# Kernel tuning notes

Measured on AMD Instinct MI355X. Metric: run time of the kernel, lower is better.

Reference implementation:

```python
import jax, jax.numpy as jnp
import numpy as np

DIM, H, C = 1024, 16, 64
D = DIM // H  # head_dim = 64
GATE_HID = 16


def setup_inputs() -> dict:
    key = jax.random.key(0)
    ks = jax.random.split(key, 8)
    B, L = 2, 2048

    def xav(k, fan_in, fan_out):
        return jax.random.normal(k, (fan_in, fan_out), jnp.float32) * np.sqrt(2.0 / (fan_in + fan_out))

    return {
        "x": jax.random.normal(ks[0], (B, L, DIM), jnp.float32),
        "Wq": xav(ks[1], DIM, DIM), "bq": jnp.zeros((DIM,), jnp.float32),
        "Wk": xav(ks[2], DIM, DIM), "bk": jnp.zeros((DIM,), jnp.float32),
        "Wv": xav(ks[3], DIM, DIM), "bv": jnp.zeros((DIM,), jnp.float32),
        "Wg1": xav(ks[4], DIM, GATE_HID), "bg1": jnp.zeros((GATE_HID,), jnp.float32),
        "Wg2": xav(ks[5], GATE_HID, H * D), "bg2": jnp.zeros((H * D,), jnp.float32),
    }


def reference(x, Wq, bq, Wk, bk, Wv, bv, Wg1, bg1, Wg2, bg2):
    B, L, dim = x.shape
    pad = (-L) % C
    if pad:
        x = jnp.pad(x, ((0, 0), (0, pad), (0, 0)))
    Lp = L + pad

    def proj(W, b):
        # (B, Lp, dim) -> (B, H, Lp, D)
        return (x @ W + b).reshape(B, Lp, H, D).transpose(0, 2, 1, 3)

    q, k, v = proj(Wq, bq), proj(Wk, bk), proj(Wv, bv)
    gate = jax.nn.sigmoid(jax.nn.silu(x @ Wg1 + bg1) @ Wg2 + bg2)
    alpha = 0.9 * gate.reshape(B, Lp, H, D).transpose(0, 2, 1, 3) + 0.1  # (B,H,Lp,D)

    # --- intra-chunk causal softmax attention (vectorized over chunks) ---
    Nc = Lp // C
    qc = q.reshape(B, H, Nc, C, D)
    kc = k.reshape(B, H, Nc, C, D)
    vc = v.reshape(B, H, Nc, C, D)
    scores = jnp.einsum('bhncd,bhnkd->bhnck', qc, kc) / np.sqrt(D).astype(np.float32)
    causal = jnp.tril(jnp.ones((C, C), bool))
    scores = jnp.where(causal, scores, -jnp.inf)
    intra = jnp.einsum('bhnck,bhnke->bhnce', jax.nn.softmax(scores, axis=-1), vc)
    intra = intra.reshape(B, H, Lp, D)

    # --- inter: gated linear-attention recurrence over the full sequence ---
    # Note: in the original code S is updated every timestep (including inside
    # chunks), so the 'inter' term at step t sees ALL tokens < t, not just
    # previous chunks.
    def step(S, inp):
        q_t, k_t, v_t, a_t = inp  # each (B, H, D)
        inter_t = jnp.einsum('bhd,bhde->bhe', q_t, S)
        S = a_t[..., None] * S + k_t[..., None] * v_t[..., None, :]
        return S, inter_t

    xs = tuple(a.transpose(2, 0, 1, 3) for a in (q, k, v, alpha))  # (Lp, B, H, D)
    S0 = jnp.zeros((B, H, D, D), x.dtype)
    _, inter = jax.lax.scan(step, S0, xs)  # (Lp, B, H, D)
    inter = inter.transpose(1, 2, 0, 3)  # (B, H, Lp, D)

    out = (inter + intra).transpose(0, 2, 1, 3).reshape(B, Lp, dim)
    return out[:, :L]
```

## Files before the change

### kernel.cpp

```cpp
#include <hip/hip_runtime.h>
#include <math.h>

#define DIMN 1024
#define NH 16
#define HD 64
#define CHK 64
#define NB 2
#define SEQ 2048
#define NTOK (NB*SEQ)
#define NCHUNK (SEQ/CHK)
#define GH 16

typedef __bf16 bf16x8 __attribute__((ext_vector_type(8)));
typedef float f32x4 __attribute__((ext_vector_type(4)));
typedef unsigned short u16x4 __attribute__((ext_vector_type(4)));

__device__ __forceinline__ unsigned short f2bf(float f) {
  union { float f; unsigned u; } a; a.f = f;
  unsigned r = a.u + 0x7FFFu + ((a.u >> 16) & 1u);
  return (unsigned short)(r >> 16);
}
__device__ __forceinline__ float bf2f(unsigned short v) {
  union { unsigned u; float f; } a; a.u = ((unsigned)v) << 16;
  return a.f;
}

__device__ __forceinline__ void gload16(const void* g, void* l) {
  __builtin_amdgcn_global_load_lds(
      (const __attribute__((address_space(1))) void*)g,
      (__attribute__((address_space(3))) void*)l, 16, 0, 0);
}

__global__ __launch_bounds__(256) void k_cast_wT(const float* __restrict__ W0,
    const float* __restrict__ W1, const float* __restrict__ W2,
    unsigned short* __restrict__ wt) {
  __shared__ float tile[64][68];
  int z = blockIdx.z;
  const float* W = z==0 ? W0 : z==1 ? W1 : W2;
  unsigned short* o = wt + (size_t)z*DIMN*DIMN;
  int k0 = blockIdx.y*64, n0 = blockIdx.x*64;
  int tr = threadIdx.x >> 4, c0 = (threadIdx.x & 15)*4;
  #pragma unroll
  for (int s = 0; s < 4; ++s) {
    int r = tr + s*16;
    *(f32x4*)&tile[r][c0] = *(const f32x4*)(W + (size_t)(k0+r)*DIMN + n0 + c0);
  }
  __syncthreads();
  #pragma unroll
  for (int s = 0; s < 4; ++s) {
    int nn = tr + s*16;
    ushort4 v;
    v.x = f2bf(tile[c0+0][nn]);
    v.y = f2bf(tile[c0+1][nn]);
    v.z = f2bf(tile[c0+2][nn]);
    v.w = f2bf(tile[c0+3][nn]);
    *(ushort4*)(o + (size_t)(n0+nn)*DIMN + k0 + c0) = v;
  }
}

__global__ __launch_bounds__(256) void k_wg1t(const float* __restrict__ Wg1,
    unsigned short* __restrict__ wg1b) {
  int idx = blockIdx.x*256 + threadIdx.x;
  int k = idx & 1023, j = idx >> 10;
  wg1b[j*DIMN + k] = f2bf(Wg1[k*GH + j]);
}

__global__ __launch_bounds__(256) void k_castx_hidden(const float* __restrict__ x,
    const unsigned short* __restrict__ wg1b, const float* __restrict__ bg1,
    unsigned short* __restrict__ xb, float* __restrict__ hid) {
  __shared__ __align__(16) unsigned short xs[16][1032];
  __shared__ float red[4][16][16];
  int tid = threadIdx.x;
  size_t base = (size_t)blockIdx.x * 16 * DIMN;
  #pragma unroll
  for (int i = 0; i < 16; ++i) {
    int idx4 = tid + i*256;
    int r = idx4 >> 8, c4 = idx4 & 255;
    f32x4 v = *(const f32x4*)(x + base + (size_t)idx4*4);
    u16x4 o;
    o[0]=f2bf(v[0]); o[1]=f2bf(v[1]); o[2]=f2bf(v[2]); o[3]=f2bf(v[3]);
    *(u16x4*)&xs[r][c4*4] = o;
    *(u16x4*)(xb + base + (size_t)idx4*4) = o;
  }
  __syncthreads();
  int l = tid & 63, w = tid >> 6;
  int lr = l & 15, kg = l >> 4;
  union FB { uint4 u; bf16x8 h; } a, b;
  f32x4 acc = {0.f,0.f,0.f,0.f};
  const unsigned short* wrow = wg1b + (size_t)lr*DIMN + w*256 + kg*8;
  #pragma unroll
  for (int kk = 0; kk < 8; ++kk) {
    a.u = *(const uint4*)&xs[lr][w*256 + kk*32 + kg*8];
    b.u = *(const uint4*)(wrow + kk*32);
    acc = __builtin_amdgcn_mfma_f32_16x16x32_bf16(a.h, b.h, acc, 0, 0, 0);
  }
  #pragma unroll
  for (int rg = 0; rg < 4; ++rg) red[w][kg*4 + rg][lr] = acc[rg];
  __syncthreads();
  {
    int m = tid >> 4, j = tid & 15;
    float s = red[0][m][j] + red[1][m][j] + red[2][m][j] + red[3][m][j];
    s += bg1[j];
    hid[(blockIdx.x*16 + m)*GH + j] = s / (1.f + expf(-s));
  }
}

__global__ __launch_bounds__(256) void k_projqkv(const unsigned short* __restrict__ xb,
    const unsigned short* __restrict__ wt,
    const float* __restrict__ b0, const float* __restrict__ b1, const float* __restrict__ b2,
    unsigned short* __restrict__ o0, unsigned short* __restrict__ o1,
    unsigned short* __restrict__ o2) {
  __shared__ unsigned short As[2][128*32];
  __shared__ unsigned short Bs[2][128*32];
  int tid = threadIdx.x;
  int wg = blockIdx.y * gridDim.x + blockIdx.x;
  int swz = (wg & 7) * 96 + (wg >> 3);
  int bx = swz % 24, by = swz / 24;
  int n3 = bx*128;
  int z = n3 >> 10;
  int n0l = n3 & 1023;
  const float* bias = z==0 ? b0 : z==1 ? b1 : b2;
  unsigned short* out = z==0 ? o0 : z==1 ? o1 : o2;
  int m0 = by*128;

  int l = tid & 63;
  int w = tid >> 6;
  int wr = w >> 1, wc = w & 1;
  int lrow = l & 15, kg = l >> 4;

  f32x4 acc[4][4] = {};

  int r0s = tid >> 2, s0s = tid & 3;
  int r1s = (tid + 256) >> 2;
  int sg0 = s0s ^ ((r0s >> 1) & 3);
  int sg1 = s0s ^ ((r1s >> 1) & 3);

  #define STAGE(buf, kt) do { \
    int kb_ = (kt)*32; \
    gload16(xb + ((size_t)(m0 + r0s)*DIMN + kb_ + sg0*8), &As[buf][tid*8]); \
    gload16(wt + ((size_t)(n3 + r0s)*DIMN + kb_ + sg0*8), &Bs[buf][tid*8]); \
    gload16(xb + ((size_t)(m0 + r1s)*DIMN + kb_ + sg1*8), &As[buf][(tid+256)*8]); \
    gload16(wt + ((size_t)(n3 + r1s)*DIMN + kb_ + sg1*8), &Bs[buf][(tid+256)*8]); \
  } while (0)

  STAGE(0, 0);
  int buf = 0;
  for (int t = 0; t < DIMN/32; ++t) {
    __syncthreads();
    if (t+1 < DIMN/32) STAGE(buf^1, t+1);
    union { uint4 u; bf16x8 h; } af[4], bfr[4];
    #pragma unroll
    for (int mf = 0; mf < 4; ++mf) {
      int r = wr*64 + mf*16 + lrow;
      int slot = kg ^ ((r >> 1) & 3);
      af[mf].u = *(const uint4*)&As[buf][r*32 + slot*8];
    }
    #pragma unroll
    for (int nf = 0; nf < 4; ++nf) {
      int r = wc*64 + nf*16 + lrow;
      int slot = kg ^ ((r >> 1) & 3);
      bfr[nf].u = *(const uint4*)&Bs[buf][r*32 + slot*8];
    }
    #pragma unroll
    for (int mf = 0; mf < 4; ++mf)
      #pragma unroll
      for (int nf = 0; nf < 4; ++nf)
        acc[mf][nf] = __builtin_amdgcn_mfma_f32_16x16x32_bf16(
            af[mf].h, bfr[nf].h, acc[mf][nf], 0, 0, 0);
    buf ^= 1;
  }
  #undef STAGE

  float bv[4];
  #pragma unroll
  for (int nf = 0; nf < 4; ++nf) bv[nf] = bias[n0l + wc*64 + nf*16 + lrow];
  #pragma unroll
  for (int mf = 0; mf < 4; ++mf) {
    int rbase = m0 + wr*64 + mf*16 + kg*4;
    #pragma unroll
    for (int nf = 0; nf < 4; ++nf) {
      int c = n0l + wc*64 + nf*16 + lrow;
      #pragma unroll
      for (int rg = 0; rg < 4; ++rg)
        out[(size_t)(rbase+rg)*DIMN + c] = f2bf(acc[mf][nf][rg] + bv[nf]);
    }
  }
}

__global__ __launch_bounds__(256) void k_ginc(const unsigned short* __restrict__ kbuf,
    const unsigned short* __restrict__ vbuf,
    const float* __restrict__ hid, const float* __restrict__ Wg2,
    const float* __restrict__ bg2,
    unsigned short* __restrict__ G, float* __restrict__ Bv) {
  __shared__ __align__(16) float kl[CHK][HD+4];
  __shared__ __align__(16) float vl[CHK][HD+4];
  __shared__ __align__(16) float al[CHK][HD+4];
  __shared__ float wprod[4][HD];
  int tid = threadIdx.x;
  int bid = blockIdx.x;
  int bh = bid >> 5, n = bid & 31;
  int b = bh >> 4, h = bh & 15;
  int colbase = h*HD;
  size_t rowbase = (size_t)b*SEQ + n*CHK;
  int dd = tid & 63, w = tid >> 6;

  float* scr = &al[0][0];
  {
    int r = tid >> 2, j0 = (tid & 3)*4;
    *(f32x4*)&scr[r*16 + j0] = *(const f32x4*)(hid + (rowbase + r)*GH + j0);
    int j = tid >> 4, d0 = (tid & 15)*4;
    *(f32x4*)&scr[1024 + j*64 + d0] = *(const f32x4*)(Wg2 + (size_t)j*DIMN + colbase + d0);
  }
  #pragma unroll
  for (int i = 0; i < 4; ++i) {
    int f4 = tid + i*256;
    int r = f4 >> 4, cg = f4 & 15;
    size_t g = (rowbase + r)*DIMN + colbase + cg*4;
    u16x4 k4 = *(const u16x4*)(kbuf + g);
    u16x4 v4 = *(const u16x4*)(vbuf + g);
    #pragma unroll
    for (int j = 0; j < 4; ++j) {
      kl[r][cg*4+j] = bf2f(k4[j]);
      vl[r][cg*4+j] = bf2f(v4[j]);
    }
  }
  __syncthreads();

  float av[16];
  {
    int r = tid >> 2, db = (tid & 3)*16;
    #pragma unroll
    for (int dq = 0; dq < 16; ++dq) {
      int d = db + dq;
      float acc = bg2[colbase + d];
      #pragma unroll
      for (int j = 0; j < GH; ++j)
        acc = fmaf(scr[r*16 + j], scr[1024 + j*64 + d], acc);
      float gg = 1.f/(1.f + expf(-acc));
      av[dq] = fmaf(0.9f, gg, 0.1f);
    }
  }
  __syncthreads();
  {
    int r = tid >> 2, db = (tid & 3)*16;
    #pragma unroll
    for (int dq = 0; dq < 16; dq += 4) {
      f32x4 v4 = {av[dq], av[dq+1], av[dq+2], av[dq+3]};
      *(f32x4*)&al[r][db + dq] = v4;
    }
  }
  __syncthreads();

  {
    float sp = 1.f;
    for (int ii = 15; ii >= 0; --ii) {
      int i = w*16 + ii;
      kl[i][dd] *= sp;
      sp *= al[i][dd];
    }
    wprod[w][dd] = sp;
  }
  __syncthreads();
  if (w < 3) {
    float tail = 1.f;
    for (int w2 = w+1; w2 < 4; ++w2) tail *= wprod[w2][dd];
    for (int ii = 0; ii < 16; ++ii) kl[w*16+ii][dd] *= tail;
  }
  if (tid < HD)
    Bv[(size_t)bid*HD + tid] = wprod[0][tid]*wprod[1][tid]*wprod[2][tid]*wprod[3][tid];
  __syncthreads();

  int ti = tid >> 4, te = tid & 15;
  int d0 = ti*4, e0 = te*4;
  float acc[4][4] = {};
  for (int i = 0; i < CHK; ++i) {
    float4 kh = *(const float4*)&kl[i][d0];
    float4 vv = *(const float4*)&vl[i][e0];
    float kf[4] = {kh.x,kh.y,kh.z,kh.w};
    float vf[4] = {vv.x,vv.y,vv.z,vv.w};
    #pragma unroll
    for (int r = 0; r < 4; ++r)
      #pragma unroll
      for (int c = 0; c < 4; ++c)
        acc[r][c] = fmaf(kf[r], vf[c], acc[r][c]);
  }
  unsigned short* gp = G + (size_t)bid*(HD*HD);
  #pragma unroll
  for (int r = 0; r < 4; ++r) {
    ushort4 o;
    o.x = f2bf(acc[r][0]); o.y = f2bf(acc[r][1]);
    o.z = f2bf(acc[r][2]); o.w = f2bf(acc[r][3]);
    *(ushort4*)(gp + (d0+r)*HD + e0) = o;
  }
}

__global__ __launch_bounds__(256) void k_scan(unsigned short* __restrict__ buf,
    const float* __restrict__ Bv) {
  int idx = blockIdx.x*256 + threadIdx.x;
  int e = idx & 63, d = (idx >> 6) & 63, bh = idx >> 12;
  unsigned short* gp = buf + (size_t)bh*NCHUNK*HD*HD + d*HD + e;
  const float* bp = Bv + (size_t)bh*NCHUNK*HD + d;
  float s = 0.f;
  float g = bf2f(gp[0]), bb = bp[0];
  #pragma unroll
  for (int n = 0; n < NCHUNK; ++n) {
    float gn = 0.f, bn = 0.f;
    if (n+1 < NCHUNK) { gn = bf2f(gp[(n+1)*(HD*HD)]); bn = bp[(n+1)*HD]; }
    gp[n*(HD*HD)] = f2bf(s);
    s = fmaf(bb, s, g);
    g = gn; bb = bn;
  }
}

__global__ __launch_bounds__(256) void k_chunk(const unsigned short* __restrict__ qbuf,
    const unsigned short* __restrict__ kbuf, const unsigned short* __restrict__ vbuf,
    const float* __restrict__ hid, const float* __restrict__ Wg2,
    const float* __restrict__ bg2,
    const unsigned short* __restrict__ states, float* __restrict__ outp) {
  __shared__ __align__(16) unsigned short qb16[64*72];
  __shared__ __align__(16) unsigned short kb16[64*72];
  __shared__ __align__(16) unsigned short vT[64*72];
  __shared__ __align__(16) unsigned short Pl[64*72];
  __shared__ __align__(16) unsigned short Swt[2][64*72];
  __shared__ __align__(16) float lb[65*68];
  __shared__ __align__(16) unsigned short dgs[4][16*40];
  __shared__ float seg[4][64];

  const int tid = threadIdx.x;
  const int bid = blockIdx.x;
  const int bh = bid >> 5, n = bid & 31;
  const int b = bh >> 4, h = bh & 15;
  const int colbase = h*HD;
  const size_t rowbase = (size_t)b*SEQ + n*CHK;
  const unsigned short* stp = states + (size_t)(bh*NCHUNK + n)*(HD*HD);

  float* scr = (float*)Pl;
  {
    int r = tid >> 2, j0 = (tid & 3)*4;
    *(f32x4*)&scr[r*16 + j0] = *(const f32x4*)(hid + (rowbase + r)*GH + j0);
    int j = tid >> 4, d0 = (tid & 15)*4;
    *(f32x4*)&scr[1024 + j*64 + d0] = *(const f32x4*)(Wg2 + (size_t)j*DIMN + colbase + d0);
  }
  #pragma unroll
  for (int i = 0; i < 4; ++i) {
    int f4 = tid + i*256;
    int r = f4 >> 4, cg = f4 & 15, c0 = cg*4;
    size_t g = (rowbase + r)*DIMN + colbase + c0;
    u16x4 q4 = *(const u16x4*)(qbuf + g);
    u16x4 k4 = *(const u16x4*)(kbuf + g);
    u16x4 v4 = *(const u16x4*)(vbuf + g);
    u16x4 s4 = *(const u16x4*)(stp + r*HD + c0);
    #pragma unroll
    for (int j = 0; j < 4; ++j) {
      vT[(c0+j)*72 + r] = v4[j];
      Swt[0][(c0+j)*72 + r] = s4[j];
    }
    *(u16x4*)&qb16[r*72 + c0] = q4;
    *(u16x4*)&kb16[r*72 + c0] = k4;
  }
  __syncthreads();

  {
    int r = tid >> 2, db = (tid & 3)*16;
    float av[16];
    #pragma unroll
    for (int dq = 0; dq < 16; ++dq) {
      int d = db + dq;
      float acc = bg2[colbase + d];
      #pragma unroll
      for (int j = 0; j < GH; ++j)
        acc = fmaf(scr[r*16 + j], scr[1024 + j*64 + d], acc);
      float gg = 1.f/(1.f + expf(-acc));
      av[dq] = log2f(fmaf(0.9f, gg, 0.1f));
    }
    #pragma unroll
    for (int dq = 0; dq < 16; dq += 4) {
      f32x4 v4 = {av[dq], av[dq+1], av[dq+2], av[dq+3]};
      *(f32x4*)&lb[r*68 + db + dq] = v4;
    }
  }
  __syncthreads();

  {
    int d = tid & 63, ww = tid >> 6;
    float run = 0.f;
    #pragma unroll
    for (int ii = 0; ii < 16; ++ii) {
      int i = ww*16 + ii;
      float t = lb[i*68 + d];
      lb[i*68 + d] = run;
      run += t;
    }
    seg[ww][d] = run;
  }
  __syncthreads();
  {
    int d = tid & 63, ww = tid >> 6;
    float carry = 0.f;
    for (int w2 = 0; w2 < ww; ++w2) carry += seg[w2][d];
    if (ww > 0)
      for (int ii = 0; ii < 16; ++ii) lb[(ww*16+ii)*68 + d] += carry;
    if (ww == 3) lb[64*68 + d] = carry + seg[3][d];
  }
  __syncthreads();

  const int l = tid & 63, w = tid >> 6;
  const int lr = l & 15, lg = l >> 4;
  const int ks = lg*8;
  const int arow = w*16 + lr;

  union FB { uint4 u; bf16x8 h; unsigned short s[8]; };

  FB qa0, qa1;
  qa0.u = *(const uint4*)&qb16[arow*72 + ks];
  qa1.u = *(const uint4*)&qb16[arow*72 + 32 + ks];
  f32x4 sc[4];
  #pragma unroll
  for (int nf = 0; nf < 4; ++nf) {
    FB b0, b1;
    b0.u = *(const uint4*)&kb16[(nf*16+lr)*72 + ks];
    b1.u = *(const uint4*)&kb16[(nf*16+lr)*72 + 32 + ks];
    f32x4 z = {0.f,0.f,0.f,0.f};
    z = __builtin_amdgcn_mfma_f32_16x16x32_bf16(qa0.h, b0.h, z, 0,0,0);
    z = __builtin_amdgcn_mfma_f32_16x16x32_bf16(qa1.h, b1.h, z, 0,0,0);
    sc[nf] = z;
  }

  float rmax[4] = {-3e38f,-3e38f,-3e38f,-3e38f};
  #pragma unroll
  for (int nf = 0; nf < 4; ++nf) {
    int col = nf*16 + lr;
    #pragma unroll
    for (int rg = 0; rg < 4; ++rg) {
      int row = w*16 + lg*4 + rg;
      float v = sc[nf][rg]*0.125f;
      if (col > row) v = -1e30f;
      sc[nf][rg] = v;
      rmax[rg] = fmaxf(rmax[rg], v);
    }
  }
  #pragma unroll
  for (int m = 1; m <= 8; m <<= 1)
    #pragma unroll
    for (int rg = 0; rg < 4; ++rg)
      rmax[rg] = fmaxf(rmax[rg], __shfl_xor(rmax[rg], m));
  float rsum[4] = {0.f,0.f,0.f,0.f};
  #pragma unroll
  for (int nf = 0; nf < 4; ++nf)
    #pragma unroll
    for (int rg = 0; rg < 4; ++rg) {
      float e = exp2f((sc[nf][rg] - rmax[rg])*1.44269504f);
      sc[nf][rg] = e;
      rsum[rg] += e;
    }
  #pragma unroll
  for (int m = 1; m <= 8; m <<= 1)
    #pragma unroll
    for (int rg = 0; rg < 4; ++rg)
      rsum[rg] += __shfl_xor(rsum[rg], m);
  __syncthreads();
  #pragma unroll
  for (int nf = 0; nf < 4; ++nf)
    #pragma unroll
    for (int rg = 0; rg < 4; ++rg)
      Pl[(w*16 + lg*4 + rg)*72 + nf*16 + lr] = f2bf(sc[nf][rg]);
  float inv[4];
  #pragma unroll
  for (int rg = 0; rg < 4; ++rg) inv[rg] = 1.f/rsum[rg];
  __syncthreads();

  f32x4 acc[4];
  {
    FB p0, p1;
    p0.u = *(const uint4*)&Pl[arow*72 + ks];
    p1.u = *(const uint4*)&Pl[arow*72 + 32 + ks];
    #pragma unroll
    for (int nf = 0; nf < 4; ++nf) {
      FB v0, v1;
      v0.u = *(const uint4*)&vT[(nf*16+lr)*72 + ks];
      v1.u = *(const uint4*)&vT[(nf*16+lr)*72 + 32 + ks];
      f32x4 z = {0.f,0.f,0.f,0.f};
      z = __builtin_amdgcn_mfma_f32_16x16x32_bf16(p0.h, v0.h, z, 0,0,0);
      z = __builtin_amdgcn_mfma_f32_16x16x32_bf16(p1.h, v1.h, z, 0,0,0);
      #pragma unroll
      for (int rg = 0; rg < 4; ++rg)
        acc[nf][rg] = z[rg]*inv[rg];
    }
  }

  {
    int dA = arow;
    float lb32 = lb[32*68 + dA];
    FB ku;
    #pragma unroll
    for (int j = 0; j < 8; ++j) {
      int s = ks + j;
      float kv = bf2f(kb16[s*72 + dA]);
      ku.s[j] = f2bf(kv * exp2f(lb32 - lb[(s+1)*68 + dA]));
    }
    int d0 = w*16 + lg*4;
    float bs[4];
    #pragma unroll
    for (int rg = 0; rg < 4; ++rg) bs[rg] = exp2f(lb[32*68 + d0 + rg]);
    #pragma unroll
    for (int nf = 0; nf < 4; ++nf) {
      int e = nf*16 + lr;
      FB vv;
      vv.u = *(const uint4*)&vT[e*72 + ks];
      f32x4 z = {0.f,0.f,0.f,0.f};
      z = __builtin_amdgcn_mfma_f32_16x16x32_bf16(ku.h, vv.h, z, 0,0,0);
      u16x4 s0v = *(const u16x4*)&Swt[0][e*72 + d0];
      u16x4 s1v;
      #pragma unroll
      for (int rg = 0; rg < 4; ++rg)
        s1v[rg] = f2bf(z[rg] + bs[rg]*bf2f(s0v[rg]));
      *(u16x4*)&Swt[1][e*72 + d0] = s1v;
    }
  }
  __syncthreads();

  {
    const int T = (w >= 2) ? 32 : 0;
    const unsigned short* Ssel = (w >= 2) ? &Swt[1][0] : &Swt[0][0];
    FB qd[2];
    #pragma unroll
    for (int kst = 0; kst < 2; ++kst) {
      int ds = kst*32 + ks;
      f32x4 lbi0 = *(const f32x4*)&lb[arow*68 + ds];
      f32x4 lbi1 = *(const f32x4*)&lb[arow*68 + ds + 4];
      f32x4 lbt0 = *(const f32x4*)&lb[T*68 + ds];
      f32x4 lbt1 = *(const f32x4*)&lb[T*68 + ds + 4];
      FB qr;
      qr.u = *(const uint4*)&qb16[arow*72 + ds];
      #pragma unroll
      for (int j = 0; j < 4; ++j) {
        qd[kst].s[j]   = f2bf(bf2f(qr.s[j])   * exp2f(lbi0[j] - lbt0[j]));
        qd[kst].s[4+j] = f2bf(bf2f(qr.s[4+j]) * exp2f(lbi1[j] - lbt1[j]));
      }
    }
    #pragma unroll
    for (int nf = 0; nf < 4; ++nf) {
      FB s0f, s1f;
      s0f.u = *(const uint4*)&Ssel[(nf*16+lr)*72 + ks];
      s1f.u = *(const uint4*)&Ssel[(nf*16+lr)*72 + 32 + ks];
      acc[nf] = __builtin_amdgcn_mfma_f32_16x16x32_bf16(qd[0].h, s0f.h, acc[nf], 0,0,0);
      acc[nf] = __builtin_amdgcn_mfma_f32_16x16x32_bf16(qd[1].h, s1f.h, acc[nf], 0,0,0);
    }
    const int nb_ = (w & 1) ? 2 : 1;
    f32x4 dgc[2] = {{0.f,0.f,0.f,0.f},{0.f,0.f,0.f,0.f}};
    #pragma unroll
    for (int bf_ = 0; bf_ < 2; ++bf_) {
      if (bf_ < nb_) {
        int s = T + bf_*16 + lr;
        f32x4 z = {0.f,0.f,0.f,0.f};
        #pragma unroll
        for (int kst = 0; kst < 2; ++kst) {
          int ds = kst*32 + ks;
          f32x4 lbt0 = *(const f32x4*)&lb[T*68 + ds];
          f32x4 lbt1 = *(const f32x4*)&lb[T*68 + ds + 4];
          f32x4 lbs0 = *(const f32x4*)&lb[(s+1)*68 + ds];
          f32x4 lbs1 = *(const f32x4*)&lb[(s+1)*68 + ds + 4];
          FB kr, kd;
          kr.u = *(const uint4*)&kb16[s*72 + ds];
          #pragma unroll
          for (int j = 0; j < 4; ++j) {
            kd.s[j]   = f2bf(bf2f(kr.s[j])   * exp2f(lbt0[j] - lbs0[j]));
            kd.s[4+j] = f2bf(bf2f(kr.s[4+j]) * exp2f(lbt1[j] - lbs1[j]));
          }
          z = __builtin_amdgcn_mfma_f32_16x16x32_bf16(qd[kst].h, kd.h, z, 0,0,0);
        }
        dgc[bf_] = z;
      }
    }
    int iis = (w & 1)*16 + lg*4;
    #pragma unroll
    for (int bf_ = 0; bf_ < 2; ++bf_) {
      #pragma unroll
      for (int rg = 0; rg < 4; ++rg) {
        int ssu = bf_*16 + lr;
        float v = (bf_ < nb_ && ssu < iis + rg) ? dgc[bf_][rg] : 0.f;
        dgs[w][(lg*4 + rg)*40 + bf_*16 + lr] = f2bf(v);
      }
    }
    FB dga;
    dga.u = *(const uint4*)&dgs[w][lr*40 + ks];
    #pragma unroll
    for (int nf = 0; nf < 4; ++nf) {
      FB vv;
      vv.u = *(const uint4*)&vT[(nf*16+lr)*72 + T + ks];
      acc[nf] = __builtin_amdgcn_mfma_f32_16x16x32_bf16(dga.h, vv.h, acc[nf], 0,0,0);
    }
  }

  #pragma unroll
  for (int nf = 0; nf < 4; ++nf)
    #pragma unroll
    for (int rg = 0; rg < 4; ++rg)
      outp[(rowbase + w*16 + lg*4 + rg)*DIMN + colbase + nf*16 + lr] = acc[nf][rg];
}

extern "C" void kernel_launch(void* const* d_in, const int* in_sizes, int n_in,
                              void* d_out, int out_size, void* d_ws, size_t ws_size,
                              hipStream_t stream) {
  const float* x   = (const float*)d_in[0];
  const float* Wq  = (const float*)d_in[1];
  const float* bq  = (const float*)d_in[2];
  const float* Wk  = (const float*)d_in[3];
  const float* bk  = (const float*)d_in[4];
  const float* Wv  = (const float*)d_in[5];
  const float* bv  = (const float*)d_in[6];
  const float* Wg1 = (const float*)d_in[7];
  const float* bg1 = (const float*)d_in[8];
  const float* Wg2 = (const float*)d_in[9];
  const float* bg2 = (const float*)d_in[10];
  float* out = (float*)d_out;

  float* ws = (float*)d_ws;
  const size_t NT = (size_t)NTOK*DIMN;
  const size_t NST = (size_t)NB*NH*NCHUNK*HD*HD;
  float* hid = ws;
  float* Bv  = hid + (size_t)NTOK*GH;
  unsigned short* stb = (unsigned short*)(Bv + (size_t)NB*NH*NCHUNK*HD);
  unsigned short* xb = stb + NST;
  unsigned short* wt = xb + NT;
  unsigned short* wg1b = wt + 3*(size_t)DIMN*DIMN;
  unsigned short* qb = wg1b + (size_t)GH*DIMN;
  unsigned short* kb = qb + NT;
  unsigned short* vb = kb + NT;

  k_cast_wT<<<dim3(16, 16, 3), 256, 0, stream>>>(Wq, Wk, Wv, wt);
  k_wg1t<<<(GH*DIMN)/256, 256, 0, stream>>>(Wg1, wg1b);
  k_castx_hidden<<<NTOK/16, 256, 0, stream>>>(x, wg1b, bg1, xb, hid);
  k_projqkv<<<dim3(24, 32), 256, 0, stream>>>(
      xb, wt, bq, bk, bv, qb, kb, vb);
  k_ginc<<<NB*NH*NCHUNK, 256, 0, stream>>>(kb, vb, hid, Wg2, bg2, stb, Bv);
  k_scan<<<(NB*NH*HD*HD)/256, 256, 0, stream>>>(stb, Bv);
  k_chunk<<<NB*NH*NCHUNK, 256, 0, stream>>>(qb, kb, vb, hid, Wg2, bg2, stb, out);
}
```

Before: 105.6 us.

## Use MFMA for chunk state outer products, log-space decay, and batched scan loads

Rewrites the per-chunk state kernel so the K^T·V chunk product runs on bf16 MFMA instructions using bf16 LDS tiles, replacing the scalar fp32 outer-product loop. Gate decay products now come from a log2-space prefix sum across four wave segments, which removes several sync-heavy serial passes. The scan kernel now issues all 32 chunk loads up front instead of prefetching one step ahead, which exposes memory-level parallelism at the cost of registers. Decay-weighted K is rounded to bf16 before the MFMA, and log/exp2 add small numeric differences.

```diff
diff --git a/kernel.cpp b/kernel.cpp
--- a/kernel.cpp
+++ b/kernel.cpp
@@ -192,19 +192,18 @@
     const float* __restrict__ hid, const float* __restrict__ Wg2,
     const float* __restrict__ bg2,
     unsigned short* __restrict__ G, float* __restrict__ Bv) {
-  __shared__ __align__(16) float kl[CHK][HD+4];
-  __shared__ __align__(16) float vl[CHK][HD+4];
-  __shared__ __align__(16) float al[CHK][HD+4];
-  __shared__ float wprod[4][HD];
+  __shared__ __align__(16) unsigned short kb16[64*72];
+  __shared__ __align__(16) unsigned short vT[64*72];
+  __shared__ __align__(16) unsigned short kdT[64*72];
+  __shared__ __align__(16) float scr[2048];
+  __shared__ float seg[4][64];
   int tid = threadIdx.x;
   int bid = blockIdx.x;
   int bh = bid >> 5, n = bid & 31;
   int b = bh >> 4, h = bh & 15;
   int colbase = h*HD;
   size_t rowbase = (size_t)b*SEQ + n*CHK;
-  int dd = tid & 63, w = tid >> 6;
-
-  float* scr = &al[0][0];
+
   {
     int r = tid >> 2, j0 = (tid & 3)*4;
     *(f32x4*)&scr[r*16 + j0] = *(const f32x4*)(hid + (rowbase + r)*GH + j0);
@@ -214,83 +213,71 @@
   #pragma unroll
   for (int i = 0; i < 4; ++i) {
     int f4 = tid + i*256;
-    int r = f4 >> 4, cg = f4 & 15;
-    size_t g = (rowbase + r)*DIMN + colbase + cg*4;
+    int r = f4 >> 4, cg = f4 & 15, c0 = cg*4;
+    size_t g = (rowbase + r)*DIMN + colbase + c0;
     u16x4 k4 = *(const u16x4*)(kbuf + g);
     u16x4 v4 = *(const u16x4*)(vbuf + g);
-    #pragma unroll
-    for (int j = 0; j < 4; ++j) {
-      kl[r][cg*4+j] = bf2f(k4[j]);
-      vl[r][cg*4+j] = bf2f(v4[j]);
-    }
-  }
-  __syncthreads();
-
-  float av[16];
-  {
-    int r = tid >> 2, db = (tid & 3)*16;
-    #pragma unroll
-    for (int dq = 0; dq < 16; ++dq) {
-      int d = db + dq;
-      float acc = bg2[colbase + d];
-      #pragma unroll
-      for (int j = 0; j < GH; ++j)
-        acc = fmaf(scr[r*16 + j], scr[1024 + j*64 + d], acc);
+    *(u16x4*)&kb16[r*72 + c0] = k4;
+    #pragma unroll
+    for (int j = 0; j < 4; ++j) vT[(c0+j)*72 + r] = v4[j];
+  }
+  __syncthreads();
+
+  {
+    int d = tid & 63, ig = tid >> 6;
+    float wcol[16];
+    #pragma unroll
+    for (int j = 0; j < 16; ++j) wcol[j] = scr[1024 + j*64 + d];
+    float bgd = bg2[colbase + d];
+    float P[16];
+    float run = 0.f;
+    #pragma unroll
+    for (int t = 0; t < 16; ++t) {
+      int i = ig*16 + t;
+      float acc = bgd;
+      #pragma unroll
+      for (int j = 0; j < 16; ++j) acc = fmaf(scr[i*16 + j], wcol[j], acc);
       float gg = 1.f/(1.f + expf(-acc));
-      av[dq] = fmaf(0.9f, gg, 0.1f);
-    }
-  }
-  __syncthreads();
-  {
-    int r = tid >> 2, db = (tid & 3)*16;
-    #pragma unroll
-    for (int dq = 0; dq < 16; dq += 4) {
-      f32x4 v4 = {av[dq], av[dq+1], av[dq+2], av[dq+3]};
-      *(f32x4*)&al[r][db + dq] = v4;
-    }
-  }
-  __syncthreads();
-
-  {
-    float sp = 1.f;
-    for (int ii = 15; ii >= 0; --ii) {
-      int i = w*16 + ii;
-      kl[i][dd] *= sp;
-      sp *= al[i][dd];
-    }
-    wprod[w][dd] = sp;
-  }
-  __syncthreads();
-  if (w < 3) {
-    float tail = 1.f;
-    for (int w2 = w+1; w2 < 4; ++w2) tail *= wprod[w2][dd];
-    for (int ii = 0; ii < 16; ++ii) kl[w*16+ii][dd] *= tail;
-  }
-  if (tid < HD)
-    Bv[(size_t)bid*HD + tid] = wprod[0][tid]*wprod[1][tid]*wprod[2][tid]*wprod[3][tid];
-  __syncthreads();
-
-  int ti = tid >> 4, te = tid & 15;
-  int d0 = ti*4, e0 = te*4;
-  float acc[4][4] = {};
-  for (int i = 0; i < CHK; ++i) {
-    float4 kh = *(const float4*)&kl[i][d0];
-    float4 vv = *(const float4*)&vl[i][e0];
-    float kf[4] = {kh.x,kh.y,kh.z,kh.w};
-    float vf[4] = {vv.x,vv.y,vv.z,vv.w};
-    #pragma unroll
-    for (int r = 0; r < 4; ++r)
-      #pragma unroll
-      for (int c = 0; c < 4; ++c)
-        acc[r][c] = fmaf(kf[r], vf[c], acc[r][c]);
-  }
+      run += log2f(fmaf(0.9f, gg, 0.1f));
+      P[t] = run;
+    }
+    seg[ig][d] = run;
+    __syncthreads();
+    float s0 = seg[0][d], s1 = seg[1][d], s2 = seg[2][d], s3 = seg[3][d];
+    float carry = (ig > 0 ? s0 : 0.f) + (ig > 1 ? s1 : 0.f) + (ig > 2 ? s2 : 0.f);
+    float Lb63 = s0 + s1 + s2 + s3;
+    if (ig == 0) Bv[(size_t)bid*HD + d] = exp2f(Lb63);
+    union { unsigned short s[16]; uint4 u[2]; } kd;
+    #pragma unroll
+    for (int t = 0; t < 16; ++t) {
+      int i = ig*16 + t;
+      float kv = bf2f(kb16[i*72 + d]);
+      kd.s[t] = f2bf(kv * exp2f(Lb63 - carry - P[t]));
+    }
+    *(uint4*)&kdT[d*72 + ig*16] = kd.u[0];
+    *(uint4*)&kdT[d*72 + ig*16 + 8] = kd.u[1];
+  }
+  __syncthreads();
+
+  int l = tid & 63, w = tid >> 6;
+  int lr = l & 15, kg = l >> 4;
+  int ks = kg*8;
+  int arow = w*16 + lr;
+  union FB { uint4 u; bf16x8 h; } a0, a1;
+  a0.u = *(const uint4*)&kdT[arow*72 + ks];
+  a1.u = *(const uint4*)&kdT[arow*72 + 32 + ks];
   unsigned short* gp = G + (size_t)bid*(HD*HD);
   #pragma unroll
-  for (int r = 0; r < 4; ++r) {
-    ushort4 o;
-    o.x = f2bf(acc[r][0]); o.y = f2bf(acc[r][1]);
-    o.z = f2bf(acc[r][2]); o.w = f2bf(acc[r][3]);
-    *(ushort4*)(gp + (d0+r)*HD + e0) = o;
+  for (int nf = 0; nf < 4; ++nf) {
+    FB b0v, b1v;
+    b0v.u = *(const uint4*)&vT[(nf*16+lr)*72 + ks];
+    b1v.u = *(const uint4*)&vT[(nf*16+lr)*72 + 32 + ks];
+    f32x4 z = {0.f,0.f,0.f,0.f};
+    z = __builtin_amdgcn_mfma_f32_16x16x32_bf16(a0.h, b0v.h, z, 0,0,0);
+    z = __builtin_amdgcn_mfma_f32_16x16x32_bf16(a1.h, b1v.h, z, 0,0,0);
+    #pragma unroll
+    for (int rg = 0; rg < 4; ++rg)
+      gp[(w*16 + kg*4 + rg)*HD + nf*16 + lr] = f2bf(z[rg]);
   }
 }
 
@@ -300,15 +287,16 @@
   int e = idx & 63, d = (idx >> 6) & 63, bh = idx >> 12;
   unsigned short* gp = buf + (size_t)bh*NCHUNK*HD*HD + d*HD + e;
   const float* bp = Bv + (size_t)bh*NCHUNK*HD + d;
+  float g[NCHUNK], bb[NCHUNK];
+  #pragma unroll
+  for (int n = 0; n < NCHUNK; ++n) g[n] = bf2f(gp[n*(HD*HD)]);
+  #pragma unroll
+  for (int n = 0; n < NCHUNK; ++n) bb[n] = bp[n*HD];
   float s = 0.f;
-  float g = bf2f(gp[0]), bb = bp[0];
   #pragma unroll
   for (int n = 0; n < NCHUNK; ++n) {
-    float gn = 0.f, bn = 0.f;
-    if (n+1 < NCHUNK) { gn = bf2f(gp[(n+1)*(HD*HD)]); bn = bp[(n+1)*HD]; }
     gp[n*(HD*HD)] = f2bf(s);
-    s = fmaf(bb, s, g);
-    g = gn; bb = bn;
+    s = fmaf(bb[n], s, g[n]);
   }
 }
 
```

Result: faster. 101.7 us (-3.8%).
